# Performance work log

Measured on AMD Instinct MI355X. Metric: run time of the kernel, lower is better.

The kernel has to match this reference:

```python
import jax, jax.numpy as jnp
import numpy as np

D_MODEL, D_QKV, N_HEADS, D_FFN = 2048, 128, 16, 8192
B, L = 2, 2048
EPS = 1e-8
ROPE_THETA = 10000.0


def _rope_cos_sin(seq_len, dim, dtype):
    # interleaved RoPE (rotary_embedding_torch default): pairs (0,1),(2,3),...
    inv_freq = ROPE_THETA ** (-jnp.arange(0, dim, 2, dtype=jnp.float32) / dim)
    ang = jnp.arange(seq_len, dtype=jnp.float32)[:, None] * inv_freq[None, :]  # [L, dim/2]
    return jnp.cos(ang).astype(dtype), jnp.sin(ang).astype(dtype)


def _apply_rope(t, cos, sin):
    # t: [b, h, l, d]; cos/sin: [l, d/2]
    t1, t2 = t[..., 0::2], t[..., 1::2]
    r1 = t1 * cos - t2 * sin
    r2 = t1 * sin + t2 * cos
    return jnp.stack([r1, r2], axis=-1).reshape(t.shape)


def setup_inputs() -> dict:
    key = jax.random.key(0)
    ks = jax.random.split(key, 5)
    d_out = D_QKV * N_HEADS * 3 + D_FFN * 2  # 22528
    return {
        "x": jax.random.normal(ks[0], (B, L, D_MODEL), dtype=jnp.float32),
        "g": jnp.ones((D_MODEL,), dtype=jnp.float32),
        "W_dense": jax.random.normal(ks[1], (d_out, D_MODEL), dtype=jnp.float32) * 0.02,
        "b_dense": jnp.zeros((d_out,), dtype=jnp.float32),
        "W_attn_out": jax.random.normal(ks[2], (D_MODEL, D_QKV * N_HEADS), dtype=jnp.float32) * 0.02,
        "W_ffn_out": jax.random.normal(ks[3], (D_MODEL, D_FFN), dtype=jnp.float32) * 0.02,
    }


def reference(x, g, W_dense, b_dense, W_attn_out, W_ffn_out):
    # RMSNorm (torch.norm variant): x / clamp(||x|| * d^-0.5, eps) * g
    norm = jnp.sqrt(jnp.sum(x * x, axis=-1, keepdims=True)) * (D_MODEL ** -0.5)
    normed = x / jnp.maximum(norm, EPS) * g

    h = jnp.einsum('bld,od->blo', normed, W_dense) + b_dense  # [B, L, 22528]
    dh = D_QKV * N_HEADS
    q, k, v, a, b_gate = jnp.split(h, [dh, 2 * dh, 3 * dh, 3 * dh + D_FFN], axis=-1)

    def to_heads(t):
        return t.reshape(B, L, N_HEADS, D_QKV).transpose(0, 2, 1, 3)  # [b,h,l,d]

    q, k, v = to_heads(q), to_heads(k), to_heads(v)
    cos, sin = _rope_cos_sin(L, D_QKV, x.dtype)
    q = _apply_rope(q, cos, sin)
    k = _apply_rope(k, cos, sin)

    scale = 1.0 / jnp.sqrt(jnp.asarray(D_QKV, dtype=x.dtype))
    scores = jnp.einsum('bhqd,bhkd->bhqk', q, k) * scale
    causal = jnp.tril(jnp.ones((L, L), dtype=bool))
    scores = jnp.where(causal, scores, jnp.asarray(-jnp.inf, dtype=scores.dtype))
    probs = jax.nn.softmax(scores, axis=-1)
    attn = jnp.einsum('bhqk,bhkd->bqhd', probs, v).reshape(B, L, dh)

    attn_out = jnp.einsum('blk,ok->blo', attn, W_attn_out)
    ffn_out = jnp.einsum('blf,of->blo', a * jax.nn.silu(b_gate), W_ffn_out)
    return x + attn_out + ffn_out
```

## Files before the change

### kernel.cpp

```cpp
#include <hip/hip_runtime.h>
#include <hip/hip_bf16.h>
#include <cmath>

typedef __bf16 bf16;
typedef __attribute__((ext_vector_type(8))) __bf16 bf16x8;
typedef __attribute__((ext_vector_type(4))) float f32x4;
typedef unsigned int u32;
typedef unsigned short u16;

#define D_MODEL 2048
#define NH 16
#define DQ 128
#define DH 2048
#define DFFN 8192
#define DOUT 22528
#define BATCH 2
#define SEQ 2048
#define NROWS 4096

__device__ __forceinline__ void gload16(const void* g, void* l) {
    __builtin_amdgcn_global_load_lds((__attribute__((address_space(1))) const void*)g,
                                     (__attribute__((address_space(3))) void*)l, 16, 0, 0);
}

__device__ __forceinline__ float bf2f(u16 u) {
    union { u32 i; float f; } c; c.i = ((u32)u) << 16; return c.f;
}

__global__ __launch_bounds__(256) void cvt_f32_bf16(const float* __restrict__ in,
                                                    bf16* __restrict__ out) {
    size_t i = ((size_t)blockIdx.x * 256 + threadIdx.x) * 8;
    float4 a = *(const float4*)(in + i);
    float4 b = *(const float4*)(in + i + 4);
    bf16x8 o;
    o[0]=(bf16)a.x; o[1]=(bf16)a.y; o[2]=(bf16)a.z; o[3]=(bf16)a.w;
    o[4]=(bf16)b.x; o[5]=(bf16)b.y; o[6]=(bf16)b.z; o[7]=(bf16)b.w;
    *(bf16x8*)(out + i) = o;
}

__global__ __launch_bounds__(256) void rmsnorm_k(const float* __restrict__ x,
                                                 const float* __restrict__ g,
                                                 bf16* __restrict__ out) {
    __shared__ float red[4];
    const int row = blockIdx.x;
    const int t = threadIdx.x;
    const float* xr = x + (size_t)row * D_MODEL;
    float4 v0 = *(const float4*)(xr + t*8);
    float4 v1 = *(const float4*)(xr + t*8 + 4);
    float ss = v0.x*v0.x + v0.y*v0.y + v0.z*v0.z + v0.w*v0.w
             + v1.x*v1.x + v1.y*v1.y + v1.z*v1.z + v1.w*v1.w;
    #pragma unroll
    for (int m = 32; m >= 1; m >>= 1) ss += __shfl_xor(ss, m);
    if ((t & 63) == 0) red[t >> 6] = ss;
    __syncthreads();
    float tot = red[0] + red[1] + red[2] + red[3];
    float norm = sqrtf(tot) * 0.022097086912079608f;
    float inv = 1.0f / fmaxf(norm, 1e-8f);
    float4 g0 = *(const float4*)(g + t*8);
    float4 g1 = *(const float4*)(g + t*8 + 4);
    bf16x8 o;
    o[0]=(bf16)(v0.x*inv*g0.x); o[1]=(bf16)(v0.y*inv*g0.y);
    o[2]=(bf16)(v0.z*inv*g0.z); o[3]=(bf16)(v0.w*inv*g0.w);
    o[4]=(bf16)(v1.x*inv*g1.x); o[5]=(bf16)(v1.y*inv*g1.y);
    o[6]=(bf16)(v1.z*inv*g1.z); o[7]=(bf16)(v1.w*inv*g1.w);
    *(bf16x8*)(out + (size_t)row * D_MODEL + t*8) = o;
}

template<int MODE>
__global__ __launch_bounds__(512, 2) void gemm256(
    const bf16* __restrict__ A, const bf16* __restrict__ B,
    int M, int N, int K, int nbx,
    const float* __restrict__ bias, bf16* __restrict__ outb,
    const float* __restrict__ addsrc, float* __restrict__ outf)
{
    __shared__ char smem[131072];
    const int tid = threadIdx.x;
    const int wid = tid >> 6, lane = tid & 63;
    const int la = lane & 15, hi = lane >> 4;
    const int wm = wid >> 2, wn = wid & 3;

    const int nwg = gridDim.x;
    const int cpx = nwg >> 3;
    const int bI = blockIdx.x;
    const int wg = (bI & 7) * cpx + (bI >> 3);
    const int bm = wg / nbx, bn = wg % nbx;
    const size_t m0 = (size_t)bm * 256, n0 = (size_t)bn * 256;

    const int lr = lane >> 3, lg = lane & 7;
    const int sg = lg ^ lr;
    const bf16* Asrc = A + (m0 + wid*8 + lr) * (size_t)K + sg*8;
    const bf16* Bsrc = B + (n0 + wid*8 + lr) * (size_t)K + sg*8;
    char* const myA = smem + wid*1024;
    char* const myB = smem + 32768 + wid*1024;

    const int pg0 = (hi ^ (la & 7)) << 4;
    const int pg1 = ((4 + hi) ^ (la & 7)) << 4;

    f32x4 acc[8][4] = {};
    const int NT = K >> 6;

    #pragma unroll
    for (int c = 0; c < 4; ++c) gload16(Asrc + (size_t)(c*64)*K, myA + c*8192);
    #pragma unroll
    for (int c = 0; c < 4; ++c) gload16(Bsrc + (size_t)(c*64)*K, myB + c*8192);

    for (int t = 0; t < NT; ++t) {
        const int buf = t & 1;
        if (t + 1 < NT) {
            const size_t k0 = (size_t)(t + 1) << 6;
            const int bo = (buf ^ 1) << 16;
            #pragma unroll
            for (int c = 0; c < 4; ++c) gload16(Asrc + (size_t)(c*64)*K + k0, myA + bo + c*8192);
            #pragma unroll
            for (int c = 0; c < 4; ++c) gload16(Bsrc + (size_t)(c*64)*K + k0, myB + bo + c*8192);
            asm volatile("s_waitcnt vmcnt(8)" ::: "memory");
        } else {
            asm volatile("s_waitcnt vmcnt(0)" ::: "memory");
        }
        __builtin_amdgcn_s_barrier();
        asm volatile("" ::: "memory");

        const char* Ab = smem + (buf << 16);
        const char* Bb = Ab + 32768;
        bf16x8 bfr[4][2];
        #pragma unroll
        for (int n = 0; n < 4; ++n) {
            const char* p = Bb + (wn*64 + n*16 + la) * 128;
            bfr[n][0] = *(const bf16x8*)(p + pg0);
            bfr[n][1] = *(const bf16x8*)(p + pg1);
        }
        #pragma unroll
        for (int qd = 0; qd < 4; ++qd) {
            bf16x8 af[2][2];
            #pragma unroll
            for (int mm = 0; mm < 2; ++mm) {
                const char* p = Ab + (wm*128 + (qd*2 + mm)*16 + la) * 128;
                af[mm][0] = *(const bf16x8*)(p + pg0);
                af[mm][1] = *(const bf16x8*)(p + pg1);
            }
            __builtin_amdgcn_s_setprio(1);
            #pragma unroll
            for (int mm = 0; mm < 2; ++mm)
                #pragma unroll
                for (int n = 0; n < 4; ++n) {
                    acc[qd*2+mm][n] = __builtin_amdgcn_mfma_f32_16x16x32_bf16(af[mm][0], bfr[n][0], acc[qd*2+mm][n], 0, 0, 0);
                    acc[qd*2+mm][n] = __builtin_amdgcn_mfma_f32_16x16x32_bf16(af[mm][1], bfr[n][1], acc[qd*2+mm][n], 0, 0, 0);
                }
            __builtin_amdgcn_s_setprio(0);
        }
        __builtin_amdgcn_s_barrier();
        asm volatile("" ::: "memory");
    }

    #pragma unroll
    for (int mf = 0; mf < 8; ++mf) {
        const size_t row = m0 + wm*128 + mf*16 + hi*4;
        #pragma unroll
        for (int nf = 0; nf < 4; ++nf) {
            const size_t col = n0 + wn*64 + nf*16 + la;
            if (MODE == 0) {
                const float bv = bias[col];
                #pragma unroll
                for (int r = 0; r < 4; ++r)
                    outb[(row + r) * N + col] = (bf16)(acc[mf][nf][r] + bv);
            } else {
                #pragma unroll
                for (int r = 0; r < 4; ++r) {
                    const size_t off = (row + r) * N + col;
                    outf[off] = addsrc[off] + acc[mf][nf][r];
                }
            }
        }
    }
}

template<int MODE>
__global__ __launch_bounds__(256) void gemm_bt(
    const bf16* __restrict__ A, const bf16* __restrict__ B,
    int M, int N, int K,
    const float* __restrict__ bias, bf16* __restrict__ outb,
    const float* __restrict__ addsrc, float* __restrict__ outf)
{
    __shared__ bf16 As[128][32];
    __shared__ bf16 Bs[128][32];
    const int tid = threadIdx.x;
    const int wid = tid >> 6, lane = tid & 63;
    const int la = lane & 15, hi = lane >> 4;
    const int m0 = blockIdx.y * 128, n0 = blockIdx.x * 128;
    const int wr = (wid >> 1) * 64, wc = (wid & 1) * 64;
    f32x4 acc[4][4] = {};
    const int idx0 = tid, idx1 = 256 + tid;
    const int r0 = idx0 >> 2, c0 = (idx0 & 3) << 3;
    const int r1 = idx1 >> 2, c1 = (idx1 & 3) << 3;
    const bf16* Ap0 = A + (size_t)(m0 + r0) * K + c0;
    const bf16* Ap1 = A + (size_t)(m0 + r1) * K + c1;
    const bf16* Bp0 = B + (size_t)(n0 + r0) * K + c0;
    const bf16* Bp1 = B + (size_t)(n0 + r1) * K + c1;
    char* asb = (char*)As + wid * 1024;
    char* bsb = (char*)Bs + wid * 1024;

    for (int k0 = 0; k0 < K; k0 += 32) {
        __syncthreads();
        gload16(Ap0 + k0, asb);
        gload16(Ap1 + k0, asb + 4096);
        gload16(Bp0 + k0, bsb);
        gload16(Bp1 + k0, bsb + 4096);
        __syncthreads();
        bf16x8 af[4], bfr[4];
        #pragma unroll
        for (int m = 0; m < 4; ++m) af[m] = *(const bf16x8*)&As[wr + m*16 + la][hi*8];
        #pragma unroll
        for (int n = 0; n < 4; ++n) bfr[n] = *(const bf16x8*)&Bs[wc + n*16 + la][hi*8];
        #pragma unroll
        for (int m = 0; m < 4; ++m)
            #pragma unroll
            for (int n = 0; n < 4; ++n)
                acc[m][n] = __builtin_amdgcn_mfma_f32_16x16x32_bf16(af[m], bfr[n], acc[m][n], 0, 0, 0);
    }

    #pragma unroll
    for (int m = 0; m < 4; ++m) {
        const int row = m0 + wr + m*16 + hi*4;
        #pragma unroll
        for (int n = 0; n < 4; ++n) {
            const int col = n0 + wc + n*16 + la;
            if (MODE == 0) {
                const float bv = bias[col];
                #pragma unroll
                for (int r = 0; r < 4; ++r)
                    outb[(size_t)(row + r) * N + col] = (bf16)(acc[m][n][r] + bv);
            } else {
                #pragma unroll
                for (int r = 0; r < 4; ++r) {
                    const size_t off = (size_t)(row + r) * N + col;
                    outf[off] = addsrc[off] + acc[m][n][r];
                }
            }
        }
    }
}

__global__ __launch_bounds__(256) void rope_table(float* __restrict__ ctab,
                                                  float* __restrict__ stab) {
    int idx = blockIdx.x * 256 + threadIdx.x;
    int l = idx >> 6, i = idx & 63;
    float inv = powf(10000.0f, -(float)i / 64.0f);
    float ang = (float)l * inv;
    float s, c;
    sincosf(ang, &s, &c);
    ctab[idx] = c; stab[idx] = s;
}

__device__ __forceinline__ u32 rope_pair(u32 u, float c, float s) {
    float t1 = bf2f((u16)(u & 0xffff));
    float t2 = bf2f((u16)(u >> 16));
    float r1 = t1 * c - t2 * s;
    float r2 = t1 * s + t2 * c;
    bf16 b1 = (bf16)r1, b2 = (bf16)r2;
    return (u32)__builtin_bit_cast(u16, b1) | ((u32)__builtin_bit_cast(u16, b2) << 16);
}

__global__ __launch_bounds__(256) void rope_qk(const bf16* __restrict__ h,
                                               const float* __restrict__ ctab,
                                               const float* __restrict__ stab,
                                               bf16* __restrict__ qb, bf16* __restrict__ kb) {
    int idx = blockIdx.x * 256 + threadIdx.x;
    int i  = idx & 63;
    int hh = (idx >> 6) & 15;
    int l  = (idx >> 10) & 2047;
    int b  = idx >> 21;
    size_t hrow = (size_t)(b * SEQ + l) * DOUT;
    float c = ctab[l*64 + i], s = stab[l*64 + i];
    u32 uq = *(const u32*)(h + hrow + hh*DQ + 2*i);
    u32 uk = *(const u32*)(h + hrow + DH + hh*DQ + 2*i);
    size_t orow = ((size_t)(b*NH + hh) * SEQ + l) * DQ + 2*i;
    *(u32*)(qb + orow) = rope_pair(uq, c, s);
    *(u32*)(kb + orow) = rope_pair(uk, c, s);
}

__global__ __launch_bounds__(256) void v_transpose(const bf16* __restrict__ h,
                                                   bf16* __restrict__ vt) {
    __shared__ u32 lds[64][68];
    const int lt = blockIdx.x, bh = blockIdx.y;
    const int b = bh >> 4, hh = bh & 15;
    const int t = threadIdx.x;
    const bf16* src = h + (size_t)(b * SEQ + lt * 64) * DOUT + 2*DH + hh * DQ;
    #pragma unroll
    for (int i = 0; i < 4; ++i) {
        int j = i*256 + t;
        int l = j >> 4, ch = j & 15;
        uint4 v = *(const uint4*)(src + (size_t)l * DOUT + ch*8);
        *(uint4*)&lds[l][ch*4] = v;
    }
    __syncthreads();
    bf16* dst = vt + (size_t)bh * DQ * SEQ + lt * 64;
    #pragma unroll
    for (int i = 0; i < 4; ++i) {
        int j = i*256 + t;
        int d = j >> 3, lc = j & 7;
        u32 out[4];
        #pragma unroll
        for (int m = 0; m < 4; ++m) {
            u32 a0 = lds[lc*8 + 2*m][d >> 1];
            u32 a1 = lds[lc*8 + 2*m + 1][d >> 1];
            u16 s0 = (d & 1) ? (u16)(a0 >> 16) : (u16)(a0 & 0xffff);
            u16 s1 = (d & 1) ? (u16)(a1 >> 16) : (u16)(a1 & 0xffff);
            out[m] = (u32)s0 | ((u32)s1 << 16);
        }
        *(uint4*)(dst + (size_t)d * SEQ + lc*8) = *(uint4*)out;
    }
}

__global__ __launch_bounds__(256) void silu_k(const bf16* __restrict__ h,
                                              bf16* __restrict__ ag) {
    size_t idx = ((size_t)blockIdx.x * 256 + threadIdx.x) * 8;
    int r = (int)(idx >> 13);
    int f = (int)(idx & 8191);
    const bf16* hr = h + (size_t)r * DOUT + 3*DH;
    bf16x8 va = *(const bf16x8*)(hr + f);
    bf16x8 vb = *(const bf16x8*)(hr + DFFN + f);
    bf16x8 o;
    #pragma unroll
    for (int j = 0; j < 8; ++j) {
        float a = (float)va[j];
        float b = (float)vb[j];
        float sil = b / (1.0f + __expf(-b));
        o[j] = (bf16)(a * sil);
    }
    *(bf16x8*)(ag + idx) = o;
}

__global__ __launch_bounds__(256) void attn_fa(const bf16* __restrict__ Q,
                                               const bf16* __restrict__ Kb,
                                               const bf16* __restrict__ Vt,
                                               bf16* __restrict__ O) {
    __shared__ bf16 Ks[64][128];
    __shared__ bf16 Vts[128][64];
    __shared__ bf16 Ps[4][16][64];
    const int qt = blockIdx.x, bh = blockIdx.y;
    const int b = bh >> 4, hh = bh & 15;
    const int tid = threadIdx.x, wid = tid >> 6, lane = tid & 63;
    const int la = lane & 15, hi = lane >> 4;
    const bf16* Qp = Q + (size_t)bh * SEQ * DQ;
    const bf16* Kp = Kb + (size_t)bh * SEQ * DQ;
    const bf16* Vp = Vt + (size_t)bh * DQ * SEQ;
    const int q0w = qt * 64 + wid * 16;

    bf16x8 qf[4];
    #pragma unroll
    for (int s = 0; s < 4; ++s)
        qf[s] = *(const bf16x8*)(Qp + (size_t)(q0w + la) * DQ + s*32 + hi*8);

    f32x4 acc_o[8] = {};
    float m_run[4] = {-1e30f, -1e30f, -1e30f, -1e30f};
    float l_run[4] = {0.f, 0.f, 0.f, 0.f};
    const float scale = 0.08838834764831845f;

    const int nk = qt + 1;
    for (int kt = 0; kt < nk; ++kt) {
        const int k0 = kt * 64;
        __syncthreads();
        #pragma unroll
        for (int i = 0; i < 4; ++i) {
            int j = i*256 + tid;
            int kr = j >> 4, jg = j & 15;
            gload16(Kp + (size_t)(k0 + kr) * DQ + ((jg ^ (kr & 7)) << 3),
                    (char*)Ks + i*4096 + wid*1024);
            int d = j >> 3, vg = j & 7;
            gload16(Vp + (size_t)d * SEQ + k0 + ((vg ^ (d & 7)) << 3),
                    (char*)Vts + i*4096 + wid*1024);
        }
        __syncthreads();

        f32x4 sacc[4] = {};
        __builtin_amdgcn_s_setprio(1);
        #pragma unroll
        for (int g = 0; g < 4; ++g) {
            const int krow = g*16 + la;
            #pragma unroll
            for (int s = 0; s < 4; ++s) {
                bf16x8 kf = *(const bf16x8*)((const char*)Ks + krow*256 + (((s*4 + hi) ^ (la & 7)) << 4));
                sacc[g] = __builtin_amdgcn_mfma_f32_16x16x32_bf16(qf[s], kf, sacc[g], 0, 0, 0);
            }
        }
        __builtin_amdgcn_s_setprio(0);

        float mnew[4];
        #pragma unroll
        for (int r = 0; r < 4; ++r) mnew[r] = m_run[r];
        #pragma unroll
        for (int g = 0; g < 4; ++g)
            #pragma unroll
            for (int r = 0; r < 4; ++r) {
                float sv = sacc[g][r] * scale;
                int qi = q0w + hi*4 + r;
                int ki = k0 + g*16 + la;
                sv = (ki <= qi) ? sv : -1e30f;
                sacc[g][r] = sv;
                mnew[r] = fmaxf(mnew[r], sv);
            }
        #pragma unroll
        for (int r = 0; r < 4; ++r) {
            float v = mnew[r];
            v = fmaxf(v, __shfl_xor(v, 1));
            v = fmaxf(v, __shfl_xor(v, 2));
            v = fmaxf(v, __shfl_xor(v, 4));
            v = fmaxf(v, __shfl_xor(v, 8));
            mnew[r] = v;
        }
        float resc[4], lsum[4];
        #pragma unroll
        for (int r = 0; r < 4; ++r) {
            resc[r] = __expf(m_run[r] - mnew[r]);
            m_run[r] = mnew[r];
            lsum[r] = 0.f;
        }
        #pragma unroll
        for (int g = 0; g < 4; ++g)
            #pragma unroll
            for (int r = 0; r < 4; ++r) {
                float p = __expf(sacc[g][r] - mnew[r]);
                sacc[g][r] = p;
                lsum[r] += p;
            }
        #pragma unroll
        for (int r = 0; r < 4; ++r) {
            float v = lsum[r];
            v += __shfl_xor(v, 1); v += __shfl_xor(v, 2);
            v += __shfl_xor(v, 4); v += __shfl_xor(v, 8);
            l_run[r] = l_run[r] * resc[r] + v;
        }
        #pragma unroll
        for (int g = 0; g < 4; ++g)
            #pragma unroll
            for (int r = 0; r < 4; ++r) {
                int prow = hi*4 + r;
                int pcol = (g*16 + la) ^ ((prow & 7) << 3);
                Ps[wid][prow][pcol] = (bf16)sacc[g][r];
            }
        #pragma unroll
        for (int n = 0; n < 8; ++n)
            #pragma unroll
            for (int r = 0; r < 4; ++r) acc_o[n][r] *= resc[r];
        __builtin_amdgcn_s_setprio(1);
        #pragma unroll
        for (int kk = 0; kk < 2; ++kk) {
            bf16x8 pf = *(const bf16x8*)((const char*)&Ps[wid][0][0] + la*128 +
                                         (((kk*32 + hi*8) ^ ((la & 7) << 3)) << 1));
            #pragma unroll
            for (int n = 0; n < 8; ++n) {
                const int vrow = n*16 + la;
                bf16x8 vf = *(const bf16x8*)((const char*)Vts + vrow*128 + (((kk*4 + hi) ^ (la & 7)) << 4));
                acc_o[n] = __builtin_amdgcn_mfma_f32_16x16x32_bf16(pf, vf, acc_o[n], 0, 0, 0);
            }
        }
        __builtin_amdgcn_s_setprio(0);
    }

    bf16* Op = O + (size_t)b * SEQ * DH + (size_t)hh * DQ;
    #pragma unroll
    for (int r = 0; r < 4; ++r) {
        int qi = q0w + hi*4 + r;
        float invl = 1.0f / l_run[r];
        #pragma unroll
        for (int n = 0; n < 8; ++n)
            Op[(size_t)qi * DH + n*16 + la] = (bf16)(acc_o[n][r] * invl);
    }
}

extern "C" void kernel_launch(void* const* d_in, const int* in_sizes, int n_in,
                              void* d_out, int out_size, void* d_ws, size_t ws_size,
                              hipStream_t stream) {
    const float* x       = (const float*)d_in[0];
    const float* g       = (const float*)d_in[1];
    const float* W_dense = (const float*)d_in[2];
    const float* b_dense = (const float*)d_in[3];
    const float* W_attn  = (const float*)d_in[4];
    const float* W_ffn   = (const float*)d_in[5];
    float* out = (float*)d_out;

    char* ws = (char*)d_ws;
    bf16* normed  = (bf16*)(ws + 0);
    bf16* Wd_b    = (bf16*)(ws + 16777216);
    bf16* Wa_b    = (bf16*)(ws + 109051904);
    bf16* Wf_b    = (bf16*)(ws + 117440512);
    bf16* h_b     = (bf16*)(ws + 150994944);
    bf16* ag_b    = (bf16*)(ws + 335544320);
    float* ctab   = (float*)(ws + 402653184);
    float* stab   = (float*)(ws + 403177472);
    bf16* q_b  = (bf16*)(ws + 16777216);
    bf16* k_b  = (bf16*)(ws + 16777216 + 16777216);
    bf16* vt_b = (bf16*)(ws + 16777216 + 33554432);
    bf16* attn_b = normed;

    cvt_f32_bf16<<<46137344/2048, 256, 0, stream>>>(W_dense, Wd_b);
    cvt_f32_bf16<<<4194304/2048, 256, 0, stream>>>(W_attn, Wa_b);
    cvt_f32_bf16<<<16777216/2048, 256, 0, stream>>>(W_ffn, Wf_b);
    rmsnorm_k<<<NROWS, 256, 0, stream>>>(x, g, normed);
    {
        dim3 grid((NROWS/256) * (DOUT/256));
        gemm256<0><<<grid, 512, 0, stream>>>(normed, Wd_b, NROWS, DOUT, D_MODEL,
                                             DOUT/256, b_dense, h_b, nullptr, nullptr);
    }
    rope_table<<<SEQ*64/256, 256, 0, stream>>>(ctab, stab);
    rope_qk<<<4194304/256, 256, 0, stream>>>(h_b, ctab, stab, q_b, k_b);
    {
        dim3 grid(SEQ/64, BATCH*NH);
        v_transpose<<<grid, 256, 0, stream>>>(h_b, vt_b);
    }
    silu_k<<<(size_t)NROWS*DFFN/8/256, 256, 0, stream>>>(h_b, ag_b);
    {
        dim3 grid(SEQ/64, BATCH*NH);
        attn_fa<<<grid, 256, 0, stream>>>(q_b, k_b, vt_b, attn_b);
    }
    {
        dim3 grid(D_MODEL/128, NROWS/128);
        gemm_bt<1><<<grid, 256, 0, stream>>>(attn_b, Wa_b, NROWS, D_MODEL, DH,
                                             nullptr, nullptr, x, out);
    }
    {
        dim3 grid(D_MODEL/128, NROWS/128);
        gemm_bt<1><<<grid, 256, 0, stream>>>(ag_b, Wf_b, NROWS, D_MODEL, DFFN,
                                             nullptr, nullptr, out, out);
    }
}
```

Baseline: 969.8 us.

## Interleave next-tile global loads with MFMA phases in dense GEMM main loop

The 256x256 dense GEMM main loop is restructured into four phases per K tile. Each phase issues a slice of the next tile's global-to-LDS loads, reads LDS fragments and runs a quarter of the MFMAs, with barriers and partial vmcnt waits in between. The aim is to spread memory traffic across the compute instead of issuing all prefetches up front, so load latency hides better behind MFMA work. In exchange it adds many more barriers per tile, which may cost synchronisation stalls. It also creates a cross-buffer ordering hazard if the waits are not placed exactly right.

Result: no change. 952.8 us (-1.8%).

```diff
diff --git a/kernel.cpp b/kernel.cpp
--- a/kernel.cpp
+++ b/kernel.cpp
@@ -66,8 +66,39 @@
     *(bf16x8*)(out + (size_t)row * D_MODEL + t*8) = o;
 }
 
+#define VMW(n)  asm volatile("s_waitcnt vmcnt(" #n ")" ::: "memory")
+#define LGK0()  asm volatile("s_waitcnt lgkmcnt(0)" ::: "memory")
+#define BARX()  { asm volatile("" ::: "memory"); __builtin_amdgcn_s_barrier(); asm volatile("" ::: "memory"); }
+
+#define SLINE_A(c_, t_) \
+    gload16(Asrc + (size_t)((c_)*64)*K + (size_t)(t_)*64, \
+            smem + (((t_)&1)<<16) + (c_)*8192 + wid*1024);
+#define SLINE_B(c_, t_) \
+    gload16(Bsrc + (size_t)((c_)*64)*K + (size_t)(t_)*64, \
+            smem + (((t_)&1)<<16) + 32768 + (c_)*8192 + wid*1024);
+
+#define PH_READS_B() \
+    _Pragma("unroll") for (int n = 0; n < 4; ++n) { \
+        const char* p_ = bb + (wn*64 + n*16 + la) * 128; \
+        bfr[n][0] = *(const bf16x8*)(p_ + pg0); \
+        bfr[n][1] = *(const bf16x8*)(p_ + pg1); }
+
+#define PH_READS_A(qd_) \
+    _Pragma("unroll") for (int mm = 0; mm < 2; ++mm) { \
+        const char* p_ = ab + (wm*128 + ((qd_)*2 + mm)*16 + la) * 128; \
+        af[mm][0] = *(const bf16x8*)(p_ + pg0); \
+        af[mm][1] = *(const bf16x8*)(p_ + pg1); }
+
+#define PH_MFMA(qd_) \
+    __builtin_amdgcn_s_setprio(1); \
+    _Pragma("unroll") for (int mm = 0; mm < 2; ++mm) \
+        _Pragma("unroll") for (int n = 0; n < 4; ++n) { \
+            acc[(qd_)*2+mm][n] = __builtin_amdgcn_mfma_f32_16x16x32_bf16(af[mm][0], bfr[n][0], acc[(qd_)*2+mm][n], 0, 0, 0); \
+            acc[(qd_)*2+mm][n] = __builtin_amdgcn_mfma_f32_16x16x32_bf16(af[mm][1], bfr[n][1], acc[(qd_)*2+mm][n], 0, 0, 0); } \
+    __builtin_amdgcn_s_setprio(0);
+
 template<int MODE>
-__global__ __launch_bounds__(512, 2) void gemm256(
+__global__ __launch_bounds__(512, 2) void gemm256f(
     const bf16* __restrict__ A, const bf16* __restrict__ B,
     int M, int N, int K, int nbx,
     const float* __restrict__ bias, bf16* __restrict__ outb,
@@ -90,8 +121,6 @@
     const int sg = lg ^ lr;
     const bf16* Asrc = A + (m0 + wid*8 + lr) * (size_t)K + sg*8;
     const bf16* Bsrc = B + (n0 + wid*8 + lr) * (size_t)K + sg*8;
-    char* const myA = smem + wid*1024;
-    char* const myB = smem + 32768 + wid*1024;
 
     const int pg0 = (hi ^ (la & 7)) << 4;
     const int pg1 = ((4 + hi) ^ (la & 7)) << 4;
@@ -99,57 +128,46 @@
     f32x4 acc[8][4] = {};
     const int NT = K >> 6;
 
-    #pragma unroll
-    for (int c = 0; c < 4; ++c) gload16(Asrc + (size_t)(c*64)*K, myA + c*8192);
-    #pragma unroll
-    for (int c = 0; c < 4; ++c) gload16(Bsrc + (size_t)(c*64)*K, myB + c*8192);
-
-    for (int t = 0; t < NT; ++t) {
-        const int buf = t & 1;
-        if (t + 1 < NT) {
-            const size_t k0 = (size_t)(t + 1) << 6;
-            const int bo = (buf ^ 1) << 16;
-            #pragma unroll
-            for (int c = 0; c < 4; ++c) gload16(Asrc + (size_t)(c*64)*K + k0, myA + bo + c*8192);
-            #pragma unroll
-            for (int c = 0; c < 4; ++c) gload16(Bsrc + (size_t)(c*64)*K + k0, myB + bo + c*8192);
-            asm volatile("s_waitcnt vmcnt(8)" ::: "memory");
-        } else {
-            asm volatile("s_waitcnt vmcnt(0)" ::: "memory");
-        }
-        __builtin_amdgcn_s_barrier();
-        asm volatile("" ::: "memory");
-
-        const char* Ab = smem + (buf << 16);
-        const char* Bb = Ab + 32768;
-        bf16x8 bfr[4][2];
-        #pragma unroll
-        for (int n = 0; n < 4; ++n) {
-            const char* p = Bb + (wn*64 + n*16 + la) * 128;
-            bfr[n][0] = *(const bf16x8*)(p + pg0);
-            bfr[n][1] = *(const bf16x8*)(p + pg1);
-        }
-        #pragma unroll
-        for (int qd = 0; qd < 4; ++qd) {
-            bf16x8 af[2][2];
-            #pragma unroll
-            for (int mm = 0; mm < 2; ++mm) {
-                const char* p = Ab + (wm*128 + (qd*2 + mm)*16 + la) * 128;
-                af[mm][0] = *(const bf16x8*)(p + pg0);
-                af[mm][1] = *(const bf16x8*)(p + pg1);
-            }
-            __builtin_amdgcn_s_setprio(1);
-            #pragma unroll
-            for (int mm = 0; mm < 2; ++mm)
-                #pragma unroll
-                for (int n = 0; n < 4; ++n) {
-                    acc[qd*2+mm][n] = __builtin_amdgcn_mfma_f32_16x16x32_bf16(af[mm][0], bfr[n][0], acc[qd*2+mm][n], 0, 0, 0);
-                    acc[qd*2+mm][n] = __builtin_amdgcn_mfma_f32_16x16x32_bf16(af[mm][1], bfr[n][1], acc[qd*2+mm][n], 0, 0, 0);
-                }
-            __builtin_amdgcn_s_setprio(0);
-        }
-        __builtin_amdgcn_s_barrier();
-        asm volatile("" ::: "memory");
+    SLINE_A(0,0); SLINE_A(2,0);
+    SLINE_B(0,0); SLINE_B(1,0);
+    SLINE_B(2,0); SLINE_B(3,0);
+    SLINE_A(1,0); SLINE_A(3,0);
+    VMW(2);
+    BARX();
+
+    bf16x8 bfr[4][2];
+    bf16x8 af[2][2];
+
+    #pragma unroll 1
+    for (int t = 0; t < NT - 1; ++t) {
+        const char* ab = smem + ((t & 1) << 16);
+        const char* bb = ab + 32768;
+        const int nx = t + 1;
+        PH_READS_B(); PH_READS_A(0);
+        SLINE_A(0,nx); SLINE_A(2,nx);
+        BARX(); LGK0(); PH_MFMA(0); BARX();
+        PH_READS_A(1);
+        SLINE_B(0,nx); SLINE_B(1,nx);
+        BARX(); LGK0(); PH_MFMA(1); VMW(4); BARX();
+        PH_READS_A(2);
+        SLINE_B(2,nx); SLINE_B(3,nx);
+        BARX(); LGK0(); PH_MFMA(2); BARX();
+        PH_READS_A(3);
+        SLINE_A(1,nx); SLINE_A(3,nx);
+        BARX(); LGK0(); PH_MFMA(3); VMW(2); BARX();
+    }
+    {
+        const int t = NT - 1;
+        const char* ab = smem + ((t & 1) << 16);
+        const char* bb = ab + 32768;
+        PH_READS_B(); PH_READS_A(0);
+        BARX(); LGK0(); PH_MFMA(0); BARX();
+        PH_READS_A(1);
+        BARX(); LGK0(); PH_MFMA(1); VMW(0); BARX();
+        PH_READS_A(2);
+        BARX(); LGK0(); PH_MFMA(2); BARX();
+        PH_READS_A(3);
+        BARX(); LGK0(); PH_MFMA(3); BARX();
     }
 
     #pragma unroll
@@ -499,8 +517,8 @@
     rmsnorm_k<<<NROWS, 256, 0, stream>>>(x, g, normed);
     {
         dim3 grid((NROWS/256) * (DOUT/256));
-        gemm256<0><<<grid, 512, 0, stream>>>(normed, Wd_b, NROWS, DOUT, D_MODEL,
-                                             DOUT/256, b_dense, h_b, nullptr, nullptr);
+        gemm256f<0><<<grid, 512, 0, stream>>>(normed, Wd_b, NROWS, DOUT, D_MODEL,
+                                              DOUT/256, b_dense, h_b, nullptr, nullptr);
     }
     rope_table<<<SEQ*64/256, 256, 0, stream>>>(ctab, stab);
     rope_qk<<<4194304/256, 256, 0, stream>>>(h_b, ctab, stab, q_b, k_b);
```
